# Kernel tuning notes

Measured on AMD Instinct MI355X. Metric: run time of the kernel, lower is better.

## Reference

```python
import jax, jax.numpy as jnp
import numpy as np

B, T, D = 2, 2048, 1024
H, W = 16, 256  # n_head, window_size
HD = D // H


def setup_inputs() -> dict:
    key = jax.random.key(0)
    ks = jax.random.split(key, 5)
    s = 0.02
    return {
        "x": jax.random.normal(ks[0], (B, T, D), dtype=jnp.float32),
        "Wqkv": jax.random.normal(ks[1], (3 * D, D), dtype=jnp.float32) * s,
        "bqkv": jax.random.normal(ks[2], (3 * D,), dtype=jnp.float32) * s,
        "Wo": jax.random.normal(ks[3], (D, D), dtype=jnp.float32) * s,
        "bo": jax.random.normal(ks[4], (D,), dtype=jnp.float32) * s,
    }


def reference(x, Wqkv, bqkv, Wo, bo):
    b, t, d = x.shape
    qkv = x @ Wqkv.T + bqkv  # [b, t, 3d]
    # rearrange 'b t (c h d) -> c b h t d'
    qkv = qkv.reshape(b, t, 3, H, HD)
    q = jnp.transpose(qkv[:, :, 0], (0, 2, 1, 3))  # [b, h, t, hd]
    k = jnp.transpose(qkv[:, :, 1], (0, 2, 1, 3))
    v = jnp.transpose(qkv[:, :, 2], (0, 2, 1, 3))
    scores = jnp.einsum('bhid,bhjd->bhij', q, k) / jnp.sqrt(jnp.float32(HD))
    i = jnp.arange(t)[:, None]
    j = jnp.arange(t)[None, :]
    # tril(diag=0) & triu(diag=-(W-1)): j <= i and j >= i - (W-1)
    mask = (j <= i) & (j >= i - (W - 1))
    scores = jnp.where(mask, scores, -jnp.inf)
    probs = jax.nn.softmax(scores, axis=-1)
    y = jnp.einsum('bhij,bhjd->bhid', probs, v)
    y = jnp.transpose(y, (0, 2, 1, 3)).reshape(b, t, d)  # b h t d -> b t (h d)
    return y @ Wo.T + bo
```

## Files before the change

### kernel.cpp

```cpp
#include <hip/hip_runtime.h>
#include <hip/hip_bf16.h>
#include <stdint.h>


typedef __attribute__((ext_vector_type(8))) short short8;
typedef __attribute__((ext_vector_type(4))) float f32x4;

#define MFMA16(a, b, c) __builtin_amdgcn_mfma_f32_16x16x32_bf16((a), (b), (c), 0, 0, 0)

static __device__ __forceinline__ void gl_lds16(const void* g, void* l) {
  __builtin_amdgcn_global_load_lds(
      (const __attribute__((address_space(1))) unsigned int*)g,
      (__attribute__((address_space(3))) unsigned int*)l, 16, 0, 0);
}

#define LGKM0 do { asm volatile("s_waitcnt lgkmcnt(0)" ::: "memory"); \
                   __builtin_amdgcn_sched_barrier(0); } while (0)
#define BARM do { asm volatile("" ::: "memory"); \
                  __builtin_amdgcn_s_barrier(); \
                  asm volatile("" ::: "memory"); } while (0)

static __device__ __forceinline__ uint32_t pkbf(float x, float y) {
  union { __hip_bfloat16 h; uint16_t u; } a, b;
  a.h = __float2bfloat16(x);
  b.h = __float2bfloat16(y);
  return (uint32_t)a.u | ((uint32_t)b.u << 16);
}

__global__ void cvt_all(const float* __restrict__ x, const float* __restrict__ wqkv,
                        const float* __restrict__ wo, __hip_bfloat16* __restrict__ xb,
                        __hip_bfloat16* __restrict__ wqkvb,
                        __hip_bfloat16* __restrict__ wob) {
  const int N0 = 524288, N1 = 393216, N2 = 131072;
  int i = blockIdx.x * blockDim.x + threadIdx.x;
  const int stride = gridDim.x * blockDim.x;
  for (; i < N0 + N1 + N2; i += stride) {
    const float* in;
    __hip_bfloat16* out;
    int gidx;
    if (i < N0) { in = x; out = xb; gidx = i; }
    else if (i < N0 + N1) { in = wqkv; out = wqkvb; gidx = i - N0; }
    else { in = wo; out = wob; gidx = i - N0 - N1; }
    const float4* p = (const float4*)in + (size_t)gidx * 2;
    float4 v0 = p[0], v1 = p[1];
    union { short8 s; __hip_bfloat16 h[8]; } u;
    u.h[0] = __float2bfloat16(v0.x); u.h[1] = __float2bfloat16(v0.y);
    u.h[2] = __float2bfloat16(v0.z); u.h[3] = __float2bfloat16(v0.w);
    u.h[4] = __float2bfloat16(v1.x); u.h[5] = __float2bfloat16(v1.y);
    u.h[6] = __float2bfloat16(v1.z); u.h[7] = __float2bfloat16(v1.w);
    ((short8*)out)[gidx] = u.s;
  }
}

__global__ __launch_bounds__(512, 4) void gemm_qkv(
    const __hip_bfloat16* __restrict__ A, const __hip_bfloat16* __restrict__ Bm,
    const float* __restrict__ bias,
    __hip_bfloat16* __restrict__ qb, __hip_bfloat16* __restrict__ kb,
    __hip_bfloat16* __restrict__ vt2) {
  __shared__ alignas(128) char smem[81920];
  const int tid = threadIdx.x;
  const int lane = tid & 63, w = tid >> 6;
  const int wm = w >> 2, wn = w & 3;
  const int r = lane & 15, g = lane >> 4;
  const int K = 1024, NT = 16;

  const int cpx = gridDim.x >> 3;
  const int swzb = (blockIdx.x & 7) * cpx + (blockIdx.x >> 3);
  const int bm = swzb >> 4, bn = swzb & 15;

  const int srow = tid >> 3;
  const int e = (tid & 7) ^ ((tid >> 4) & 7);
  const int koff = (e >> 2) * 32 + (e & 3) * 8;
  const __hip_bfloat16* aU[2];
  const __hip_bfloat16* bU[3];
#pragma unroll
  for (int U = 0; U < 2; ++U)
    aU[U] = A + (size_t)(bm * 128 + U * 64 + srow) * K + koff;
#pragma unroll
  for (int U = 0; U < 3; ++U)
    bU[U] = Bm + (size_t)(bn * 192 + U * 64 + srow) * K + koff;
  const int ldst = tid * 16;

#define STA(t, U) gl_lds16(aU[U] + (t) * 64, smem + ((t) & 1) * 40960 + (U) * 8192 + ldst)
#define STB(t, U) gl_lds16(bU[U] + (t) * 64, smem + ((t) & 1) * 40960 + 16384 + (U) * 8192 + ldst)

  const int hsw = (r >> 1) & 7;
  const int s0 = ((0 + g) ^ hsw) * 16;
  const int s1 = ((4 + g) ^ hsw) * 16;
  const int rdA = (wm * 64 + r) * 128;
  const int rdB = 16384 + (wn * 48 + r) * 128;

  f32x4 acc[4][3] = {};
  short8 af[4][2], bf[3][2];

  STA(0, 0); STA(0, 1); STB(0, 0); STB(0, 1); STB(0, 2);
  STA(1, 0); STA(1, 1); STB(1, 0); STB(1, 1); STB(1, 2);
  asm volatile("s_waitcnt vmcnt(5)" ::: "memory");
  BARM;

#pragma unroll 1
  for (int t = 0; t < NT; ++t) {
    const char* cb = smem + (t & 1) * 40960;
#pragma unroll
    for (int i = 0; i < 2; ++i) {
      af[i][0] = *(const short8*)(cb + rdA + i * 2048 + s0);
      af[i][1] = *(const short8*)(cb + rdA + i * 2048 + s1);
    }
#pragma unroll
    for (int j = 0; j < 3; ++j) {
      bf[j][0] = *(const short8*)(cb + rdB + j * 2048 + s0);
      bf[j][1] = *(const short8*)(cb + rdB + j * 2048 + s1);
    }
    BARM;
    LGKM0;
    __builtin_amdgcn_s_setprio(1);
#pragma unroll
    for (int i = 0; i < 2; ++i)
#pragma unroll
      for (int j = 0; j < 3; ++j) acc[i][j] = MFMA16(af[i][0], bf[j][0], acc[i][j]);
#pragma unroll
    for (int i = 0; i < 2; ++i)
#pragma unroll
      for (int j = 0; j < 3; ++j) acc[i][j] = MFMA16(af[i][1], bf[j][1], acc[i][j]);
    __builtin_amdgcn_s_setprio(0);
    BARM;
#pragma unroll
    for (int i = 0; i < 2; ++i) {
      af[i + 2][0] = *(const short8*)(cb + rdA + (i + 2) * 2048 + s0);
      af[i + 2][1] = *(const short8*)(cb + rdA + (i + 2) * 2048 + s1);
    }
    if (t + 2 < NT) { STB(t + 2, 0); STB(t + 2, 1); STB(t + 2, 2); }
    BARM;
    LGKM0;
    __builtin_amdgcn_s_setprio(1);
#pragma unroll
    for (int i = 0; i < 2; ++i)
#pragma unroll
      for (int j = 0; j < 3; ++j) acc[i + 2][j] = MFMA16(af[i + 2][0], bf[j][0], acc[i + 2][j]);
#pragma unroll
    for (int i = 0; i < 2; ++i)
#pragma unroll
      for (int j = 0; j < 3; ++j) acc[i + 2][j] = MFMA16(af[i + 2][1], bf[j][1], acc[i + 2][j]);
    __builtin_amdgcn_s_setprio(0);
    BARM;
    if (t + 2 < NT) {
      STA(t + 2, 0); STA(t + 2, 1);
      asm volatile("s_waitcnt vmcnt(5)" ::: "memory");
    } else if (t + 1 < NT) {
      asm volatile("s_waitcnt vmcnt(0)" ::: "memory");
    }
    BARM;
  }
#undef STA
#undef STB

  float bjv[3];
  const int nb = bn * 192 + wn * 48;
#pragma unroll
  for (int j = 0; j < 3; ++j) bjv[j] = bias[nb + j * 16 + r];
#pragma unroll
  for (int i = 0; i < 4; ++i) {
    const int m0 = bm * 128 + wm * 64 + i * 16 + g * 4;
#pragma unroll
    for (int j = 0; j < 3; ++j) {
      const int nn = nb + j * 16 + r;
      const int c = nn >> 10, h = (nn >> 6) & 15, hd = nn & 63;
      const int b_ = m0 >> 11, t0 = m0 & 2047;
      const size_t hb = (size_t)(b_ * 16 + h);
      if (c == 0) {
#pragma unroll
        for (int q = 0; q < 4; ++q)
          qb[(hb * 2048 + t0 + q) * 64 + hd] =
              __float2bfloat16((acc[i][j][q] + bjv[j]) * 0.125f);
      } else if (c == 1) {
#pragma unroll
        for (int q = 0; q < 4; ++q)
          kb[(hb * 2048 + t0 + q) * 64 + hd] =
              __float2bfloat16(acc[i][j][q] + bjv[j]);
      } else {
        union { uint2 u; __hip_bfloat16 hh[4]; } pk;
#pragma unroll
        for (int q = 0; q < 4; ++q)
          pk.hh[q] = __float2bfloat16(acc[i][j][q] + bjv[j]);
        const int kk = t0 & 31;
        const int pp = ((kk & 12) << 1) + ((kk & 16) >> 2);
        *(uint2*)&vt2[hb * 131072 + (size_t)(t0 >> 5) * 2048 + hd * 32 + pp] =
            pk.u;
      }
    }
  }
}

__global__ __launch_bounds__(512, 4) void gemm_out8(
    const __hip_bfloat16* __restrict__ A, const __hip_bfloat16* __restrict__ Bm,
    const float* __restrict__ bias, float* __restrict__ outF) {
  __shared__ alignas(128) char smem[65536];
  const int tid = threadIdx.x;
  const int lane = tid & 63, w = tid >> 6;
  const int wm = w >> 2, wn = w & 3;
  const int r = lane & 15, g = lane >> 4;
  const int K = 1024, NT = 16;

  const int cpx = gridDim.x >> 3;
  const int swzb = (blockIdx.x & 7) * cpx + (blockIdx.x >> 3);
  const int bm = swzb >> 3, bn = swzb & 7;

  const int srow = tid >> 3;
  const int e = (tid & 7) ^ ((tid >> 4) & 7);
  const int koff = (e >> 2) * 32 + (e & 3) * 8;
  const __hip_bfloat16* aU[2];
  const __hip_bfloat16* bU[2];
#pragma unroll
  for (int U = 0; U < 2; ++U) {
    aU[U] = A + (size_t)(bm * 128 + U * 64 + srow) * K + koff;
    bU[U] = Bm + (size_t)(bn * 128 + U * 64 + srow) * K + koff;
  }
  const int ldst = tid * 16;

#define STA(t, U) gl_lds16(aU[U] + (t) * 64, smem + ((t) & 1) * 32768 + (U) * 8192 + ldst)
#define STB(t, U) gl_lds16(bU[U] + (t) * 64, smem + ((t) & 1) * 32768 + 16384 + (U) * 8192 + ldst)

  const int hsw = (r >> 1) & 7;
  const int s0 = ((0 + g) ^ hsw) * 16;
  const int s1 = ((4 + g) ^ hsw) * 16;
  const int rdA = (wm * 64 + r) * 128;
  const int rdB = 16384 + (wn * 32 + r) * 128;

  f32x4 acc[4][2] = {};
  short8 af[4][2], bf[2][2];

  STA(0, 0); STA(0, 1); STB(0, 0); STB(0, 1);
  STA(1, 0); STA(1, 1); STB(1, 0); STB(1, 1);
  asm volatile("s_waitcnt vmcnt(4)" ::: "memory");
  BARM;

#pragma unroll 1
  for (int t = 0; t < NT; ++t) {
    const char* cb = smem + (t & 1) * 32768;
#pragma unroll
    for (int i = 0; i < 2; ++i) {
      af[i][0] = *(const short8*)(cb + rdA + i * 2048 + s0);
      af[i][1] = *(const short8*)(cb + rdA + i * 2048 + s1);
    }
#pragma unroll
    for (int j = 0; j < 2; ++j) {
      bf[j][0] = *(const short8*)(cb + rdB + j * 2048 + s0);
      bf[j][1] = *(const short8*)(cb + rdB + j * 2048 + s1);
    }
    BARM;
    LGKM0;
    __builtin_amdgcn_s_setprio(1);
#pragma unroll
    for (int i = 0; i < 2; ++i)
#pragma unroll
      for (int j = 0; j < 2; ++j) acc[i][j] = MFMA16(af[i][0], bf[j][0], acc[i][j]);
#pragma unroll
    for (int i = 0; i < 2; ++i)
#pragma unroll
      for (int j = 0; j < 2; ++j) acc[i][j] = MFMA16(af[i][1], bf[j][1], acc[i][j]);
    __builtin_amdgcn_s_setprio(0);
    BARM;
#pragma unroll
    for (int i = 0; i < 2; ++i) {
      af[i + 2][0] = *(const short8*)(cb + rdA + (i + 2) * 2048 + s0);
      af[i + 2][1] = *(const short8*)(cb + rdA + (i + 2) * 2048 + s1);
    }
    if (t + 2 < NT) { STB(t + 2, 0); STB(t + 2, 1); }
    BARM;
    LGKM0;
    __builtin_amdgcn_s_setprio(1);
#pragma unroll
    for (int i = 0; i < 2; ++i)
#pragma unroll
      for (int j = 0; j < 2; ++j) acc[i + 2][j] = MFMA16(af[i + 2][0], bf[j][0], acc[i + 2][j]);
#pragma unroll
    for (int i = 0; i < 2; ++i)
#pragma unroll
      for (int j = 0; j < 2; ++j) acc[i + 2][j] = MFMA16(af[i + 2][1], bf[j][1], acc[i + 2][j]);
    __builtin_amdgcn_s_setprio(0);
    BARM;
    if (t + 2 < NT) {
      STA(t + 2, 0); STA(t + 2, 1);
      asm volatile("s_waitcnt vmcnt(4)" ::: "memory");
    } else if (t + 1 < NT) {
      asm volatile("s_waitcnt vmcnt(0)" ::: "memory");
    }
    BARM;
  }
#undef STA
#undef STB

  float bjv[2];
  const int nb = bn * 128 + wn * 32;
#pragma unroll
  for (int j = 0; j < 2; ++j) bjv[j] = bias[nb + j * 16 + r];
#pragma unroll
  for (int i = 0; i < 4; ++i) {
    const int m0 = bm * 128 + wm * 64 + i * 16 + g * 4;
#pragma unroll
    for (int j = 0; j < 2; ++j) {
      const int nn = nb + j * 16 + r;
#pragma unroll
      for (int q = 0; q < 4; ++q)
        outF[(size_t)(m0 + q) * 1024 + nn] = acc[i][j][q] + bjv[j];
    }
  }
}

__global__ __launch_bounds__(512, 2) void attn_local(
    const __hip_bfloat16* __restrict__ qb, const __hip_bfloat16* __restrict__ kb,
    const __hip_bfloat16* __restrict__ vt2, __hip_bfloat16* __restrict__ yb) {
  __shared__ alignas(16) char smem[49152];
  const int xcd = blockIdx.x & 7;
  const int idx = blockIdx.x >> 3;
  const int bh = xcd + (idx >> 4) * 8;
  const int qt = idx & 15;
  const int tid = threadIdx.x;
  const int w = tid >> 6, lane = tid & 63;
  const int r = lane & 15, g = lane >> 4;
  const int qa = qt * 128 + w * 16;

  const __hip_bfloat16* qp = qb + (size_t)bh * 2048 * 64;
  const __hip_bfloat16* kp = kb + (size_t)bh * 2048 * 64;
  const __hip_bfloat16* vpb = vt2 + (size_t)bh * 131072 + r * 32 + g * 8;

  const int t_lo = (qt >= 2) ? (4 * qt - 8) : 0;
  const int t_hi = 4 * qt + 3;
  const int nunits = (t_hi - t_lo + 1) << 8;
  short8 stg[6];
#pragma unroll
  for (int rr = 0; rr < 6; ++rr) {
    const int u = rr * 512 + tid;
    if (u < nunits) {
      const int tt = u >> 8, row = (u >> 3) & 31, sl = u & 7;
      stg[rr] = *(const short8*)&kp[(size_t)((t_lo + tt) * 32 + row) * 64 + sl * 8];
    }
  }
#pragma unroll
  for (int rr = 0; rr < 6; ++rr) {
    const int u = rr * 512 + tid;
    if (u < nunits) {
      const int tt = u >> 8, row = (u >> 3) & 31, sl = u & 7;
      *(short8*)(smem + tt * 4096 + row * 128 + ((sl ^ (row & 7)) << 4)) = stg[rr];
    }
  }
  __syncthreads();

  const short8 qf0 = *(const short8*)&qp[(qa + r) * 64 + g * 8];
  const short8 qf1 = *(const short8*)&qp[(qa + r) * 64 + g * 8 + 32];

  f32x4 acc[4] = {};
  float m = -1e30f;
  float lsum = 0.f;

  const int wlo = ((qa >= 256) ? ((qa - 255) >> 5) : 0) - t_lo;
  const int whi = ((qa + 15) >> 5) - t_lo;
  const int xsw = (r & 7) << 4;

#pragma unroll 1
  for (int tt = wlo; tt <= whi; ++tt) {
    const int tabs = t_lo + tt;
    const int kbase = tabs << 5;
    const short8 v0 = *(const short8*)(vpb + (size_t)tabs * 2048);
    const short8 v1 = *(const short8*)(vpb + (size_t)tabs * 2048 + 512);
    const short8 v2 = *(const short8*)(vpb + (size_t)tabs * 2048 + 1024);
    const short8 v3 = *(const short8*)(vpb + (size_t)tabs * 2048 + 1536);
    const char* kt = smem + tt * 4096;
    const short8 k00 = *(const short8*)(kt + r * 128 + (((g) << 4) ^ xsw));
    const short8 k01 = *(const short8*)(kt + r * 128 + (((4 + g) << 4) ^ xsw));
    const short8 k10 = *(const short8*)(kt + (16 + r) * 128 + (((g) << 4) ^ xsw));
    const short8 k11 = *(const short8*)(kt + (16 + r) * 128 + (((4 + g) << 4) ^ xsw));
    f32x4 st0 = {}, st1 = {};
    st0 = MFMA16(k00, qf0, st0);
    st0 = MFMA16(k01, qf1, st0);
    st1 = MFMA16(k10, qf0, st1);
    st1 = MFMA16(k11, qf1, st1);
    float sv[2][4];
#pragma unroll
    for (int q = 0; q < 4; ++q) {
      const unsigned d0 = (unsigned)(qa + r) - (unsigned)(kbase + g * 4 + q);
      const unsigned d1 = (unsigned)(qa + r) - (unsigned)(kbase + 16 + g * 4 + q);
      sv[0][q] = (d0 <= 255u) ? st0[q] : -1e30f;
      sv[1][q] = (d1 <= 255u) ? st1[q] : -1e30f;
    }
    const float tmax = fmaxf(
        fmaxf(fmaxf(sv[0][0], sv[0][1]), fmaxf(sv[0][2], sv[0][3])),
        fmaxf(fmaxf(sv[1][0], sv[1][1]), fmaxf(sv[1][2], sv[1][3])));
    if (!__all(tmax <= m + 8.f)) {
      float rm = tmax;
      rm = fmaxf(rm, __shfl_xor(rm, 16));
      rm = fmaxf(rm, __shfl_xor(rm, 32));
      const float mnew = fmaxf(m, rm);
      const float fac = __expf(m - mnew);
      m = mnew;
      lsum *= fac;
      acc[0] *= fac; acc[1] *= fac; acc[2] *= fac; acc[3] *= fac;
    }
    float p[2][4];
#pragma unroll
    for (int f = 0; f < 2; ++f)
#pragma unroll
      for (int q = 0; q < 4; ++q) {
        p[f][q] = __expf(sv[f][q] - m);
        lsum += p[f][q];
      }
    union { short8 s; uint32_t u[4]; } pb;
    pb.u[0] = pkbf(p[0][0], p[0][1]);
    pb.u[1] = pkbf(p[0][2], p[0][3]);
    pb.u[2] = pkbf(p[1][0], p[1][1]);
    pb.u[3] = pkbf(p[1][2], p[1][3]);
    acc[0] = MFMA16(v0, pb.s, acc[0]);
    acc[1] = MFMA16(v1, pb.s, acc[1]);
    acc[2] = MFMA16(v2, pb.s, acc[2]);
    acc[3] = MFMA16(v3, pb.s, acc[3]);
  }

  lsum += __shfl_xor(lsum, 16);
  lsum += __shfl_xor(lsum, 32);
  const float inv = 1.f / lsum;

  const int b_ = bh >> 4, h = bh & 15;
  __hip_bfloat16* yrow = yb + (size_t)(b_ * 2048 + qa + r) * 1024 + h * 64;
#pragma unroll
  for (int u = 0; u < 4; ++u) {
    union { uint2 uu; __hip_bfloat16 hh[4]; } pk;
#pragma unroll
    for (int q = 0; q < 4; ++q) pk.hh[q] = __float2bfloat16(acc[u][q] * inv);
    *(uint2*)&yrow[u * 16 + g * 4] = pk.uu;
  }
}

extern "C" void kernel_launch(void* const* d_in, const int* in_sizes, int n_in,
                              void* d_out, int out_size, void* d_ws,
                              size_t ws_size, hipStream_t stream) {
  const float* x = (const float*)d_in[0];
  const float* Wqkv = (const float*)d_in[1];
  const float* bqkv = (const float*)d_in[2];
  const float* Wo = (const float*)d_in[3];
  const float* bo = (const float*)d_in[4];
  float* out = (float*)d_out;

  char* ws = (char*)d_ws;
  __hip_bfloat16* xb = (__hip_bfloat16*)(ws + 0);
  __hip_bfloat16* wqkvb = (__hip_bfloat16*)(ws + 8388608);
  __hip_bfloat16* wob = (__hip_bfloat16*)(ws + 14680064);
  __hip_bfloat16* qb = (__hip_bfloat16*)(ws + 16777216);
  __hip_bfloat16* kb = (__hip_bfloat16*)(ws + 25165824);
  __hip_bfloat16* vt2 = (__hip_bfloat16*)(ws + 33554432);
  __hip_bfloat16* yb = (__hip_bfloat16*)(ws + 41943040);

  cvt_all<<<2048, 256, 0, stream>>>(x, Wqkv, Wo, xb, wqkvb, wob);

  gemm_qkv<<<512, 512, 0, stream>>>(xb, wqkvb, bqkv, qb, kb, vt2);
  attn_local<<<512, 512, 0, stream>>>(qb, kb, vt2, yb);
  gemm_out8<<<256, 512, 0, stream>>>(yb, wob, bo, out);
}
```

Before: 72.11 us.

## Merge GEMM half-phases, stage attention K via direct LDS loads, raise occupancy

The two GEMM kernels load all A fragments at once and run every MFMA in a single phase, removing two barriers per k-step. Global-to-LDS prefetch for both A and B is issued after the compute. The attention kernel loads K tiles with global_load_lds, applying the swizzle on the source address, and sets priority around the MFMAs. Its launch bound rises to 6 waves per EU, which limits registers and may cause spills, and prefetch now overlaps less with compute.

```diff
diff --git a/kernel.cpp b/kernel.cpp
--- a/kernel.cpp
+++ b/kernel.cpp
@@ -102,7 +102,7 @@
   for (int t = 0; t < NT; ++t) {
     const char* cb = smem + (t & 1) * 40960;
 #pragma unroll
-    for (int i = 0; i < 2; ++i) {
+    for (int i = 0; i < 4; ++i) {
       af[i][0] = *(const short8*)(cb + rdA + i * 2048 + s0);
       af[i][1] = *(const short8*)(cb + rdA + i * 2048 + s1);
     }
@@ -111,39 +111,20 @@
       bf[j][0] = *(const short8*)(cb + rdB + j * 2048 + s0);
       bf[j][1] = *(const short8*)(cb + rdB + j * 2048 + s1);
     }
-    BARM;
     LGKM0;
     __builtin_amdgcn_s_setprio(1);
 #pragma unroll
-    for (int i = 0; i < 2; ++i)
+    for (int i = 0; i < 4; ++i)
 #pragma unroll
       for (int j = 0; j < 3; ++j) acc[i][j] = MFMA16(af[i][0], bf[j][0], acc[i][j]);
 #pragma unroll
-    for (int i = 0; i < 2; ++i)
+    for (int i = 0; i < 4; ++i)
 #pragma unroll
       for (int j = 0; j < 3; ++j) acc[i][j] = MFMA16(af[i][1], bf[j][1], acc[i][j]);
     __builtin_amdgcn_s_setprio(0);
     BARM;
-#pragma unroll
-    for (int i = 0; i < 2; ++i) {
-      af[i + 2][0] = *(const short8*)(cb + rdA + (i + 2) * 2048 + s0);
-      af[i + 2][1] = *(const short8*)(cb + rdA + (i + 2) * 2048 + s1);
-    }
-    if (t + 2 < NT) { STB(t + 2, 0); STB(t + 2, 1); STB(t + 2, 2); }
-    BARM;
-    LGKM0;
-    __builtin_amdgcn_s_setprio(1);
-#pragma unroll
-    for (int i = 0; i < 2; ++i)
-#pragma unroll
-      for (int j = 0; j < 3; ++j) acc[i + 2][j] = MFMA16(af[i + 2][0], bf[j][0], acc[i + 2][j]);
-#pragma unroll
-    for (int i = 0; i < 2; ++i)
-#pragma unroll
-      for (int j = 0; j < 3; ++j) acc[i + 2][j] = MFMA16(af[i + 2][1], bf[j][1], acc[i + 2][j]);
-    __builtin_amdgcn_s_setprio(0);
-    BARM;
     if (t + 2 < NT) {
+      STB(t + 2, 0); STB(t + 2, 1); STB(t + 2, 2);
       STA(t + 2, 0); STA(t + 2, 1);
       asm volatile("s_waitcnt vmcnt(5)" ::: "memory");
     } else if (t + 1 < NT) {
@@ -238,7 +219,7 @@
   for (int t = 0; t < NT; ++t) {
     const char* cb = smem + (t & 1) * 32768;
 #pragma unroll
-    for (int i = 0; i < 2; ++i) {
+    for (int i = 0; i < 4; ++i) {
       af[i][0] = *(const short8*)(cb + rdA + i * 2048 + s0);
       af[i][1] = *(const short8*)(cb + rdA + i * 2048 + s1);
     }
@@ -247,39 +228,20 @@
       bf[j][0] = *(const short8*)(cb + rdB + j * 2048 + s0);
       bf[j][1] = *(const short8*)(cb + rdB + j * 2048 + s1);
     }
-    BARM;
     LGKM0;
     __builtin_amdgcn_s_setprio(1);
 #pragma unroll
-    for (int i = 0; i < 2; ++i)
+    for (int i = 0; i < 4; ++i)
 #pragma unroll
       for (int j = 0; j < 2; ++j) acc[i][j] = MFMA16(af[i][0], bf[j][0], acc[i][j]);
 #pragma unroll
-    for (int i = 0; i < 2; ++i)
+    for (int i = 0; i < 4; ++i)
 #pragma unroll
       for (int j = 0; j < 2; ++j) acc[i][j] = MFMA16(af[i][1], bf[j][1], acc[i][j]);
     __builtin_amdgcn_s_setprio(0);
     BARM;
-#pragma unroll
-    for (int i = 0; i < 2; ++i) {
-      af[i + 2][0] = *(const short8*)(cb + rdA + (i + 2) * 2048 + s0);
-      af[i + 2][1] = *(const short8*)(cb + rdA + (i + 2) * 2048 + s1);
-    }
-    if (t + 2 < NT) { STB(t + 2, 0); STB(t + 2, 1); }
-    BARM;
-    LGKM0;
-    __builtin_amdgcn_s_setprio(1);
-#pragma unroll
-    for (int i = 0; i < 2; ++i)
-#pragma unroll
-      for (int j = 0; j < 2; ++j) acc[i + 2][j] = MFMA16(af[i + 2][0], bf[j][0], acc[i + 2][j]);
-#pragma unroll
-    for (int i = 0; i < 2; ++i)
-#pragma unroll
-      for (int j = 0; j < 2; ++j) acc[i + 2][j] = MFMA16(af[i + 2][1], bf[j][1], acc[i + 2][j]);
-    __builtin_amdgcn_s_setprio(0);
-    BARM;
     if (t + 2 < NT) {
+      STB(t + 2, 0); STB(t + 2, 1);
       STA(t + 2, 0); STA(t + 2, 1);
       asm volatile("s_waitcnt vmcnt(4)" ::: "memory");
     } else if (t + 1 < NT) {
@@ -307,7 +269,7 @@
   }
 }
 
-__global__ __launch_bounds__(512, 2) void attn_local(
+__global__ __launch_bounds__(512, 6) void attn_local(
     const __hip_bfloat16* __restrict__ qb, const __hip_bfloat16* __restrict__ kb,
     const __hip_bfloat16* __restrict__ vt2, __hip_bfloat16* __restrict__ yb) {
   __shared__ alignas(16) char smem[49152];
@@ -327,27 +289,21 @@
   const int t_lo = (qt >= 2) ? (4 * qt - 8) : 0;
   const int t_hi = 4 * qt + 3;
   const int nunits = (t_hi - t_lo + 1) << 8;
-  short8 stg[6];
 #pragma unroll
   for (int rr = 0; rr < 6; ++rr) {
     const int u = rr * 512 + tid;
     if (u < nunits) {
       const int tt = u >> 8, row = (u >> 3) & 31, sl = u & 7;
-      stg[rr] = *(const short8*)&kp[(size_t)((t_lo + tt) * 32 + row) * 64 + sl * 8];
-    }
-  }
-#pragma unroll
-  for (int rr = 0; rr < 6; ++rr) {
-    const int u = rr * 512 + tid;
-    if (u < nunits) {
-      const int tt = u >> 8, row = (u >> 3) & 31, sl = u & 7;
-      *(short8*)(smem + tt * 4096 + row * 128 + ((sl ^ (row & 7)) << 4)) = stg[rr];
-    }
-  }
-  __syncthreads();
+      gl_lds16(kp + (size_t)((t_lo + tt) * 32 + row) * 64 + (sl ^ (row & 7)) * 8,
+               smem + u * 16);
+    }
+  }
 
   const short8 qf0 = *(const short8*)&qp[(qa + r) * 64 + g * 8];
   const short8 qf1 = *(const short8*)&qp[(qa + r) * 64 + g * 8 + 32];
+
+  asm volatile("s_waitcnt vmcnt(0)" ::: "memory");
+  __syncthreads();
 
   f32x4 acc[4] = {};
   float m = -1e30f;
@@ -371,10 +327,12 @@
     const short8 k10 = *(const short8*)(kt + (16 + r) * 128 + (((g) << 4) ^ xsw));
     const short8 k11 = *(const short8*)(kt + (16 + r) * 128 + (((4 + g) << 4) ^ xsw));
     f32x4 st0 = {}, st1 = {};
+    __builtin_amdgcn_s_setprio(1);
     st0 = MFMA16(k00, qf0, st0);
     st0 = MFMA16(k01, qf1, st0);
     st1 = MFMA16(k10, qf0, st1);
     st1 = MFMA16(k11, qf1, st1);
+    __builtin_amdgcn_s_setprio(0);
     float sv[2][4];
 #pragma unroll
     for (int q = 0; q < 4; ++q) {
@@ -409,10 +367,12 @@
     pb.u[1] = pkbf(p[0][2], p[0][3]);
     pb.u[2] = pkbf(p[1][0], p[1][1]);
     pb.u[3] = pkbf(p[1][2], p[1][3]);
+    __builtin_amdgcn_s_setprio(1);
     acc[0] = MFMA16(v0, pb.s, acc[0]);
     acc[1] = MFMA16(v1, pb.s, acc[1]);
     acc[2] = MFMA16(v2, pb.s, acc[2]);
     acc[3] = MFMA16(v3, pb.s, acc[3]);
+    __builtin_amdgcn_s_setprio(0);
   }
 
   lsum += __shfl_xor(lsum, 16);
```

Measured after the change: 72.47 us. About the same (+0.5%).
